# Kernel tuning notes

Hardware: AMD Instinct MI355X
Metric: run time of the kernel (lower is better)

Reference implementation:

```python
import jax, jax.numpy as jnp
import numpy as np

H = 16          # n_self_heads
CHUNK = 256     # chunk_size in chunk_gate_retention
GLN = 16.0      # gate_logit_normalizer
EPS = 1e-5      # norm_eps


def _rope_interleaved(t, cos, sin):
    # t: [B,T,H,hd]; cos,sin: [T,hd//2]; interleaved pairs (even, odd)
    x1 = t[..., 0::2]
    x2 = t[..., 1::2]
    c = cos[None, :, None, :]
    s = sin[None, :, None, :]
    r1 = x1 * c - x2 * s
    r2 = x1 * s + x2 * c
    return jnp.stack([r1, r2], axis=-1).reshape(t.shape)


def setup_inputs() -> dict:
    key = jax.random.key(0)
    ks = jax.random.split(key, 8)
    B, T, D = 2, 4096, 2048
    hd = D // H
    sc = D ** -0.5
    x = jax.random.normal(ks[0], (B, T, D), jnp.float32)
    # real rotary tables (interleaved), [T, hd//2]
    inv_freq = 1.0 / (10000.0 ** (np.arange(0, hd, 2, dtype=np.float32) / hd))
    ang = np.outer(np.arange(T, dtype=np.float32), inv_freq)
    cos = jnp.asarray(np.cos(ang))
    sin = jnp.asarray(np.sin(ang))
    Wq = jax.random.normal(ks[1], (D, D), jnp.float32) * sc
    Wk = jax.random.normal(ks[2], (D, D), jnp.float32) * sc
    Wv = jax.random.normal(ks[3], (D, D), jnp.float32) * sc
    Wg = jax.random.normal(ks[4], (D, D), jnp.float32) * sc
    Wgt = jax.random.normal(ks[5], (D, H), jnp.float32) * sc
    Wout = jax.random.normal(ks[6], (D, D), jnp.float32) * sc
    return {"x": x, "cos": cos, "sin": sin, "Wq": Wq, "Wk": Wk, "Wv": Wv,
            "Wg": Wg, "Wgt": Wgt, "Wout": Wout}


def reference(x, cos, sin, Wq, Wk, Wv, Wg, Wgt, Wout):
    B, T, D = x.shape
    hd = D // H
    N = T // CHUNK
    scale = hd ** -0.5

    q = (x @ Wq).reshape(B, T, H, hd)
    k = (x @ Wk).reshape(B, T, H, hd)
    v = (x @ Wv).reshape(B, T, H, hd)
    g = x @ Wg                                   # [B,T,D] swiglu gate
    gt = jax.nn.log_sigmoid(x @ Wgt) / GLN       # [B,T,H] log-decay per head

    q = _rope_interleaved(q, cos, sin)
    k = _rope_interleaved(k, cos, sin)

    # chunk: [B,H,N,C,hd]
    def chunked(t):
        return t.transpose(0, 2, 1, 3).reshape(B, H, N, CHUNK, hd)
    qc, kc, vc = chunked(q), chunked(k), chunked(v)

    gtc = gt.transpose(0, 2, 1).reshape(B, H, N, CHUNK).astype(jnp.float32)
    gcum = jnp.cumsum(gtc, axis=-1)              # inclusive cumsum within chunk

    # intra-chunk: A[i,j] = (q_i.k_j)*scale * exp(gcum_i - gcum_j), j <= i
    mask = jnp.tril(jnp.ones((CHUNK, CHUNK), bool))
    dec = jnp.where(mask, jnp.exp(gcum[..., :, None] - gcum[..., None, :]), 0.0).astype(x.dtype)
    scores = jnp.einsum('bhncd,bhnsd->bhncs', qc * scale, kc) * dec
    o_inner = jnp.einsum('bhncs,bhnsd->bhncd', scores, vc)

    # cross-chunk recurrent state: S <- S*exp(g_total) + (k*exp(g_total-gcum))^T V * scale
    g_tot = gcum[..., -1:]                       # [B,H,N,1]
    k_dec = jnp.exp(g_tot - gcum).astype(x.dtype)
    S_in = jnp.einsum('bhncd,bhnce->bhnde', kc * k_dec[..., None] * scale, vc)  # [B,H,N,hd,hd]
    q_dec = jnp.exp(gcum).astype(x.dtype)        # [B,H,N,C]
    chunk_dec = jnp.exp(gcum[..., -1]).astype(x.dtype)  # [B,H,N]

    def step(S, inp):
        qcn, qd, Sin, cd = inp
        o_cross = jnp.einsum('bhcd,bhde->bhce', qcn * qd[..., None], S)
        S_new = S * cd[..., None, None] + Sin
        return S_new, o_cross

    xs = (jnp.moveaxis(qc, 2, 0), jnp.moveaxis(q_dec, 2, 0),
          jnp.moveaxis(S_in, 2, 0), jnp.moveaxis(chunk_dec, 2, 0))
    S0 = jnp.zeros((B, H, hd, hd), x.dtype)
    _, o_cross = jax.lax.scan(step, S0, xs)      # [N,B,H,C,hd]

    o = o_inner + jnp.moveaxis(o_cross, 0, 2)    # [B,H,N,C,hd]
    # RMSNorm over head_dim, no affine
    o = o * jax.lax.rsqrt(jnp.mean(o * o, axis=-1, keepdims=True) + EPS)
    o = o.reshape(B, H, T, hd).transpose(0, 2, 1, 3).reshape(B, T, D)
    o = jax.nn.silu(g) * o                       # swiglu(g, o)
    return o @ Wout
```

## Files before the change

### kernel.cpp

```cpp
#include <hip/hip_runtime.h>

typedef unsigned short u16;
typedef short bf16x8 __attribute__((ext_vector_type(8)));
typedef unsigned short u16x8 __attribute__((ext_vector_type(8)));
typedef unsigned short u16x4 __attribute__((ext_vector_type(4)));
typedef float f32x4 __attribute__((ext_vector_type(4)));

typedef __attribute__((address_space(1))) void* gas_ptr;
typedef __attribute__((address_space(3))) void* las_ptr;

__device__ __forceinline__ float bf2f(u16 v) {
  unsigned u = ((unsigned)v) << 16;
  return __builtin_bit_cast(float, u);
}
__device__ __forceinline__ u16 f2bf(float f) {
  unsigned u = __builtin_bit_cast(unsigned, f);
  u += 0x7fffu + ((u >> 16) & 1u);
  return (u16)(u >> 16);
}
__device__ __forceinline__ f32x4 mfma16(bf16x8 a, bf16x8 b, f32x4 c) {
  return __builtin_amdgcn_mfma_f32_16x16x32_bf16(a, b, c, 0, 0, 0);
}
__device__ __forceinline__ void gload_lds16(const void* g, void* l) {
  __builtin_amdgcn_global_load_lds((gas_ptr)g, (las_ptr)l, 16, 0, 0);
}

#define SB __builtin_amdgcn_sched_barrier(0)
#define BAR do { SB; __builtin_amdgcn_s_barrier(); SB; } while (0)
#define LGK do { asm volatile("s_waitcnt lgkmcnt(0)" ::: "memory"); SB; } while (0)

__global__ void k_cast(const float* __restrict__ in, u16* __restrict__ out, int n8) {
  int stride = gridDim.x * blockDim.x;
  for (int i = blockIdx.x * blockDim.x + threadIdx.x; i < n8; i += stride) {
    size_t base = (size_t)i * 8;
    f32x4 a = *(const f32x4*)(in + base);
    f32x4 b = *(const f32x4*)(in + base + 4);
    u16x8 o;
    o[0] = f2bf(a[0]); o[1] = f2bf(a[1]); o[2] = f2bf(a[2]); o[3] = f2bf(a[3]);
    o[4] = f2bf(b[0]); o[5] = f2bf(b[1]); o[6] = f2bf(b[2]); o[7] = f2bf(b[3]);
    *(u16x8*)(out + base) = o;
  }
}

__global__ __launch_bounds__(256) void k_wtrans(const float* __restrict__ W, u16* __restrict__ WT,
                                                int K, int N) {
  int n0 = blockIdx.x * 64, k0 = blockIdx.y * 64;
  int tid = threadIdx.x;
  __shared__ __align__(16) float tf[64][68];
  int r = tid >> 4, c4 = (tid & 15) * 4;
#pragma unroll
  for (int i = 0; i < 4; ++i) {
    int row = r + i * 16;
    f32x4 v = *(const f32x4*)(W + (size_t)(k0 + row) * N + n0 + c4);
    *(f32x4*)&tf[row][c4] = v;
  }
  __syncthreads();
#pragma unroll
  for (int i = 0; i < 2; ++i) {
    int chunk = tid + i * 256;
    int nl = chunk >> 3, c8 = (chunk & 7) * 8;
    u16x8 o;
#pragma unroll
    for (int m = 0; m < 8; ++m) o[m] = f2bf(tf[c8 + m][nl]);
    *(u16x8*)(WT + (size_t)(n0 + nl) * K + k0 + c8) = o;
  }
}

template <int MODE>
__global__ __launch_bounds__(512, 2) void k_gemm2(const u16* __restrict__ A,
                                                  const u16* __restrict__ Bt,
                                                  void* __restrict__ Cp, int M, int N, int K) {
  __shared__ __align__(16) u16 Al[2][2][8192];
  __shared__ __align__(16) u16 Bl[2][2][8192];
  int tid = threadIdx.x, w = tid >> 6, lane = tid & 63, l15 = lane & 15, l4 = lane >> 4;
  int wm = w >> 2, wn = w & 3;
  int nwg = gridDim.x, bid = blockIdx.x;
  int q8 = nwg >> 3;
  int wg = (bid & 7) * q8 + (bid >> 3);
  int nbx = N >> 8;
  int nstx = nbx >> 2;
  int st = wg >> 4, r16 = wg & 15;
  int sm = st / nstx, sn = st - sm * nstx;
  int m0 = ((sm << 2) + (r16 >> 2)) << 8;
  int n0 = ((sn << 2) + (r16 & 3)) << 8;
  int rA0, rA1, rB0, rB1, cc0, cc1;
  {
    int rr[2], cch[2];
#pragma unroll
    for (int q = 0; q < 2; ++q) {
      int L = (q * 512 + tid) * 16;
      int sub = L >> 10, inner = L & 1023;
      inner ^= ((inner >> 9) & 1) << 5;
      rr[q] = ((sub >> 1) << 4) + (inner >> 6);
      cch[q] = ((sub & 1) << 5) + ((inner & 63) >> 1);
    }
    rA0 = ((rr[0] >> 6) << 7) + (rr[0] & 63);
    rA1 = ((rr[1] >> 6) << 7) + (rr[1] & 63);
    rB0 = ((rr[0] >> 5) << 6) + (rr[0] & 31);
    rB1 = ((rr[1] >> 5) << 6) + (rr[1] & 31);
    cc0 = cch[0]; cc1 = cch[1];
  }
  int innerA = ((l15 << 6) + (l4 << 4)) ^ ((l15 & 8) << 2);
  int ldsW = w << 9;

#define STAGE_A(t, h)                                                                   \
  do {                                                                                  \
    int b_ = (t) & 1;                                                                   \
    gload_lds16(A + (size_t)(m0 + rA0 + (h) * 64) * K + (t) * 64 + cc0, &Al[b_][h][ldsW]); \
    gload_lds16(A + (size_t)(m0 + rA1 + (h) * 64) * K + (t) * 64 + cc1, &Al[b_][h][4096 + ldsW]); \
  } while (0)
#define STAGE_B(t, h)                                                                   \
  do {                                                                                  \
    int b_ = (t) & 1;                                                                   \
    gload_lds16(Bt + (size_t)(n0 + rB0 + (h) * 32) * K + (t) * 64 + cc0, &Bl[b_][h][ldsW]); \
    gload_lds16(Bt + (size_t)(n0 + rB1 + (h) * 32) * K + (t) * 64 + cc1, &Bl[b_][h][4096 + ldsW]); \
  } while (0)

  const f32x4 z4 = {0.f, 0.f, 0.f, 0.f};
  f32x4 acc[8][4];
#pragma unroll
  for (int i = 0; i < 8; ++i)
#pragma unroll
    for (int j = 0; j < 4; ++j) acc[i][j] = z4;
  bf16x8 af[4][2], bfr[2][2];

#define LDA(cur, hm)                                                                     \
  do {                                                                                   \
    const char* Ab = (const char*)&Al[cur][hm][0];                                       \
    _Pragma("unroll") for (int fi = 0; fi < 4; ++fi) _Pragma("unroll") for (int ks = 0; ks < 2; ++ks) \
        af[fi][ks] = *(const bf16x8*)(Ab + (((wm * 4 + fi) * 2 + ks) << 10) + innerA);   \
  } while (0)
#define LDB(cur, hn)                                                                     \
  do {                                                                                   \
    const char* Bb = (const char*)&Bl[cur][hn][0];                                       \
    _Pragma("unroll") for (int fj = 0; fj < 2; ++fj) _Pragma("unroll") for (int ks = 0; ks < 2; ++ks) \
        bfr[fj][ks] = *(const bf16x8*)(Bb + (((wn * 2 + fj) * 2 + ks) << 10) + innerA);  \
  } while (0)
#define MM(hm, hn)                                                                       \
  do {                                                                                   \
    __builtin_amdgcn_s_setprio(1);                                                       \
    _Pragma("unroll") for (int fi = 0; fi < 4; ++fi) _Pragma("unroll") for (int fj = 0; fj < 2; ++fj) \
        _Pragma("unroll") for (int ks = 0; ks < 2; ++ks)                                 \
            acc[(hm) * 4 + fi][(hn) * 2 + fj] =                                          \
                mfma16(af[fi][ks], bfr[fj][ks], acc[(hm) * 4 + fi][(hn) * 2 + fj]);      \
    __builtin_amdgcn_s_setprio(0);                                                       \
  } while (0)
#define GATE8 do { asm volatile("s_waitcnt vmcnt(8)" ::: "memory"); SB; } while (0)
#define GATE0 do { asm volatile("s_waitcnt vmcnt(0)" ::: "memory"); SB; } while (0)

  int nt = K >> 6;
  STAGE_A(0, 0); STAGE_B(0, 0); STAGE_A(0, 1); STAGE_B(0, 1);
  if (nt > 1) {
    STAGE_A(1, 0); STAGE_B(1, 0);
    asm volatile("s_waitcnt vmcnt(4)" ::: "memory");
  } else {
    asm volatile("s_waitcnt vmcnt(0)" ::: "memory");
  }
  SB;
  BAR;
  for (int t = 0; t < nt; ++t) {
    int cur = t & 1;
    bool tail = (t >= nt - 2);
    LDA(cur, 0); LDB(cur, 0);
    if (t + 1 < nt) STAGE_B(t + 1, 1);
    asm volatile("s_waitcnt lgkmcnt(8)" ::: "memory");
    BAR; LGK;
    MM(0, 0);
    if (tail) GATE0; else GATE8;
    BAR;
    LDB(cur, 1);
    if (t + 1 < nt) STAGE_A(t + 1, 1);
    BAR; LGK;
    MM(0, 1);
    if (tail) GATE0; else GATE8;
    BAR;
    LDA(cur, 1); LDB(cur, 0);
    if (t + 2 < nt) STAGE_A(t + 2, 0);
    asm volatile("s_waitcnt lgkmcnt(8)" ::: "memory");
    BAR; LGK;
    MM(1, 0);
    BAR;
    LDB(cur, 1);
    if (t + 2 < nt) STAGE_B(t + 2, 0);
    BAR; LGK;
    MM(1, 1);
    if (tail) GATE0; else GATE8;
    BAR;
  }
  asm volatile("s_waitcnt vmcnt(0)" ::: "memory");
#undef STAGE_A
#undef STAGE_B
#undef LDA
#undef LDB
#undef MM
#undef GATE8
#undef GATE0
#pragma unroll
  for (int fi = 0; fi < 8; ++fi)
#pragma unroll
    for (int fj = 0; fj < 4; ++fj) {
      int row = m0 + wm * 128 + fi * 16 + l4 * 4;
      int col = n0 + wn * 64 + fj * 16 + l15;
      if (MODE == 1) {
        float* C = (float*)Cp;
#pragma unroll
        for (int reg = 0; reg < 4; ++reg) C[(size_t)(row + reg) * N + col] = acc[fi][fj][reg];
      } else {
        u16* C = (u16*)Cp + (size_t)(col >> 11) * 16777216 + (col & 2047);
#pragma unroll
        for (int reg = 0; reg < 4; ++reg) C[(size_t)(row + reg) * 2048] = f2bf(acc[fi][fj][reg]);
      }
    }
}

__global__ __launch_bounds__(256) void k_gt(const float* __restrict__ x, const float* __restrict__ Wgt,
                                            float* __restrict__ gt) {
  int t = blockIdx.x, tid = threadIdx.x;
  __shared__ __align__(16) float xs[2048];
#pragma unroll
  for (int i = 0; i < 8; ++i) xs[tid + i * 256] = x[(size_t)t * 2048 + tid + i * 256];
  __syncthreads();
  int head = tid & 15, ks = tid >> 4;
  float p = 0.f;
  for (int i = 0; i < 128; ++i) {
    int k = ks + i * 16;
    p += xs[k] * Wgt[k * 16 + head];
  }
  __shared__ float ps[16][17];
  ps[ks][head] = p;
  __syncthreads();
  if (tid < 16) {
    float z = 0.f;
#pragma unroll
    for (int j = 0; j < 16; ++j) z += ps[j][tid];
    float lsz = (z >= 0.f) ? -log1pf(__expf(-z)) : (z - log1pf(__expf(z)));
    int b = t >> 12, tl = t & 4095;
    gt[((size_t)(b * 16 + tid)) * 4096 + tl] = lsz * 0.0625f;
  }
}

__global__ void k_cumsum(const float* __restrict__ gt, float* __restrict__ gcum) {
  int n = blockIdx.x, bh = blockIdx.y, c = threadIdx.x;
  __shared__ float s[256];
  size_t base = (size_t)bh * 4096 + n * 256;
  s[c] = gt[base + c];
  __syncthreads();
  for (int off = 1; off < 256; off <<= 1) {
    float t = (c >= off) ? s[c - off] : 0.f;
    __syncthreads();
    s[c] += t;
    __syncthreads();
  }
  gcum[base + c] = s[c];
}

__global__ void k_rope(u16* __restrict__ q, u16* __restrict__ k,
                       const float* __restrict__ cosT, const float* __restrict__ sinT) {
  const size_t total = (size_t)8192 * 512;
  size_t stride = (size_t)gridDim.x * blockDim.x;
  for (size_t idx = (size_t)blockIdx.x * blockDim.x + threadIdx.x; idx < total; idx += stride) {
    size_t tok = idx >> 9;
    int g4 = (int)(idx & 511);
    int col = g4 * 4;
    int i0 = (col & 127) >> 1;
    int tl = (int)(tok & 4095);
    float c0 = cosT[tl * 64 + i0], s0 = sinT[tl * 64 + i0];
    float c1 = cosT[tl * 64 + i0 + 1], s1 = sinT[tl * 64 + i0 + 1];
    size_t base = tok * 2048 + col;
    u16x4 qv = *(u16x4*)(q + base);
    float a0 = bf2f(qv[0]), a1 = bf2f(qv[1]), a2 = bf2f(qv[2]), a3 = bf2f(qv[3]);
    u16x4 qo;
    qo[0] = f2bf(a0 * c0 - a1 * s0); qo[1] = f2bf(a0 * s0 + a1 * c0);
    qo[2] = f2bf(a2 * c1 - a3 * s1); qo[3] = f2bf(a2 * s1 + a3 * c1);
    *(u16x4*)(q + base) = qo;
    u16x4 kv = *(u16x4*)(k + base);
    float b0 = bf2f(kv[0]), b1 = bf2f(kv[1]), b2 = bf2f(kv[2]), b3 = bf2f(kv[3]);
    u16x4 ko;
    ko[0] = f2bf(b0 * c0 - b1 * s0); ko[1] = f2bf(b0 * s0 + b1 * c0);
    ko[2] = f2bf(b2 * c1 - b3 * s1); ko[3] = f2bf(b2 * s1 + b3 * c1);
    *(u16x4*)(k + base) = ko;
  }
}

__global__ __launch_bounds__(256) void k_sin(const u16* __restrict__ kb, const u16* __restrict__ vb,
                                             const float* __restrict__ gcum, float* __restrict__ SinT) {
  int n = blockIdx.x, bh = blockIdx.y;
  int b = bh >> 4, h = bh & 15;
  int tid = threadIdx.x, w = tid >> 6, lane = tid & 63, l15 = lane & 15, l4 = lane >> 4;
  size_t t0 = (size_t)b * 4096 + n * 256;
  __shared__ float gc[256];
  __shared__ __align__(16) u16 kt[128 * 72];
  __shared__ __align__(16) u16 vt[128 * 72];
  gc[tid] = gcum[(size_t)bh * 4096 + n * 256 + tid];
  __syncthreads();
  float gtot = gc[255];
  const float scale = 0.08838834764831845f;
  const f32x4 z4 = {0.f, 0.f, 0.f, 0.f};
  f32x4 acc[2][8];
#pragma unroll
  for (int i = 0; i < 2; ++i)
#pragma unroll
    for (int j = 0; j < 8; ++j) acc[i][j] = z4;
  int cl = tid >> 2, fq = (tid & 3) * 32;
  for (int c0 = 0; c0 < 256; c0 += 64) {
    __syncthreads();
    float kd = __expf(gtot - gc[c0 + cl]) * scale;
    const u16* kp = kb + (t0 + c0 + cl) * 2048 + h * 128 + fq;
    const u16* vp = vb + (t0 + c0 + cl) * 2048 + h * 128 + fq;
#pragma unroll
    for (int jj = 0; jj < 4; ++jj) {
      u16x8 kv = *(const u16x8*)(kp + jj * 8);
      u16x8 vv = *(const u16x8*)(vp + jj * 8);
#pragma unroll
      for (int m = 0; m < 8; ++m) {
        int f = fq + jj * 8 + m;
        kt[f * 72 + cl] = f2bf(bf2f(kv[m]) * kd);
        vt[f * 72 + cl] = vv[m];
      }
    }
    __syncthreads();
#pragma unroll
    for (int ks = 0; ks < 2; ++ks) {
      int coff = ks * 32 + l4 * 8;
      bf16x8 bfr[8];
#pragma unroll
      for (int bc = 0; bc < 8; ++bc) bfr[bc] = *(const bf16x8*)(vt + (bc * 16 + l15) * 72 + coff);
#pragma unroll
      for (int ar = 0; ar < 2; ++ar) {
        bf16x8 afr = *(const bf16x8*)(kt + (w * 32 + ar * 16 + l15) * 72 + coff);
#pragma unroll
        for (int bc = 0; bc < 8; ++bc) acc[ar][bc] = mfma16(afr, bfr[bc], acc[ar][bc]);
      }
    }
  }
  size_t sbo = ((size_t)bh * 16 + n) * 16384;
#pragma unroll
  for (int ar = 0; ar < 2; ++ar) {
    int d = w * 32 + ar * 16 + l4 * 4;
#pragma unroll
    for (int bc = 0; bc < 8; ++bc) {
      int e = bc * 16 + l15;
      *(f32x4*)(SinT + sbo + (size_t)e * 128 + d) = acc[ar][bc];
    }
  }
}

__global__ void k_state(const float* __restrict__ SinT, const float* __restrict__ gcum,
                        u16* __restrict__ S_T) {
  int bh = blockIdx.x >> 3, sl = blockIdx.x & 7;
  int base_l = sl * 2048 + threadIdx.x;
  float S[8];
#pragma unroll
  for (int i = 0; i < 8; ++i) S[i] = 0.f;
  for (int nn = 0; nn < 16; ++nn) {
    size_t tb = ((size_t)bh * 16 + nn) * 16384;
#pragma unroll
    for (int i = 0; i < 8; ++i) S_T[tb + base_l + i * 256] = f2bf(S[i]);
    float cd = __expf(gcum[(size_t)bh * 4096 + nn * 256 + 255]);
#pragma unroll
    for (int i = 0; i < 8; ++i) S[i] = S[i] * cd + SinT[tb + base_l + i * 256];
  }
}

__global__ __launch_bounds__(512, 4) void k_attn(
    const u16* __restrict__ qb, const u16* __restrict__ kb, const u16* __restrict__ vb,
    const u16* __restrict__ gbuf, const float* __restrict__ gcum,
    const u16* __restrict__ S_T, u16* __restrict__ ob) {
  int n = blockIdx.x, bh = blockIdx.y;
  int b = bh >> 4, h = bh & 15;
  int tid = threadIdx.x, w = tid >> 6, lane = tid & 63, l15 = lane & 15, l4 = lane >> 4;
  size_t t0 = (size_t)b * 4096 + n * 256;
  __shared__ float gc[256];
  __shared__ __align__(16) u16 vt[32768];
  __shared__ __align__(16) u16 Pb[8][512];
  if (tid < 256) gc[tid] = gcum[(size_t)bh * 4096 + n * 256 + tid];
  {
    int s = tid & 255, e0 = (tid >> 8) * 64;
    const u16* vp = vb + (t0 + s) * 2048 + h * 128 + e0;
#pragma unroll
    for (int j = 0; j < 8; ++j) {
      u16x8 vv = *(const u16x8*)(vp + j * 8);
#pragma unroll
      for (int m = 0; m < 8; ++m) {
        int e = e0 + j * 8 + m;
        vt[(e * 256 + s) ^ ((e & 7) << 3)] = vv[m];
      }
    }
  }
  __syncthreads();
  const float scale = 0.08838834764831845f;
  u16* P = Pb[w];
  const f32x4 z4 = {0.f, 0.f, 0.f, 0.f};
  f32x4 acc[2][8];
#pragma unroll
  for (int i = 0; i < 2; ++i)
#pragma unroll
    for (int j = 0; j < 8; ++j) acc[i][j] = z4;
  int r0s[2], nsbs[2];
  r0s[0] = w * 16;        nsbs[0] = (w + 2) >> 1;
  r0s[1] = (15 - w) * 16; nsbs[1] = 8 - (w >> 1);
#pragma unroll
  for (int rb = 0; rb < 2; ++rb) {
    int r0 = r0s[rb], nsb = nsbs[rb];
    bf16x8 qa[4];
    {
      const u16* qp = qb + (t0 + r0 + l15) * 2048 + h * 128 + l4 * 8;
#pragma unroll
      for (int ks = 0; ks < 4; ++ks) qa[ks] = *(const bf16x8*)(qp + ks * 32);
    }
    for (int sbk = 0; sbk < nsb; ++sbk) {
      int s0 = sbk * 32;
      f32x4 sc[2] = {z4, z4};
#pragma unroll
      for (int cf = 0; cf < 2; ++cf) {
        const u16* kp = kb + (t0 + s0 + cf * 16 + l15) * 2048 + h * 128 + l4 * 8;
#pragma unroll
        for (int ks = 0; ks < 4; ++ks)
          sc[cf] = mfma16(qa[ks], *(const bf16x8*)(kp + ks * 32), sc[cf]);
      }
#pragma unroll
      for (int cf = 0; cf < 2; ++cf) {
        int s = s0 + cf * 16 + l15;
        float gs = gc[s];
#pragma unroll
        for (int reg = 0; reg < 4; ++reg) {
          int rl = l4 * 4 + reg;
          int r = r0 + rl;
          float val = (r >= s) ? sc[cf][reg] * scale * __expf(gc[r] - gs) : 0.f;
          P[(rl * 32 + cf * 16 + l15) ^ ((rl & 3) << 3)] = f2bf(val);
        }
      }
      bf16x8 pa = *(const bf16x8*)(P + ((l15 * 32 + l4 * 8) ^ ((l15 & 3) << 3)));
#pragma unroll
      for (int bc = 0; bc < 8; ++bc) {
        int e = bc * 16 + l15;
        bf16x8 vf = *(const bf16x8*)(vt + ((e * 256 + s0 + l4 * 8) ^ ((e & 7) << 3)));
        acc[rb][bc] = mfma16(pa, vf, acc[rb][bc]);
      }
    }
  }
  size_t sbase = ((size_t)bh * 16 + n) * 16384;
#pragma unroll
  for (int rb = 0; rb < 2; ++rb) {
    int r0 = r0s[rb];
    float qd = __expf(gc[r0 + l15]);
#pragma unroll
    for (int ks = 0; ks < 4; ++ks) {
      u16x8 qu = *(const u16x8*)(qb + (t0 + r0 + l15) * 2048 + h * 128 + ks * 32 + l4 * 8);
      u16x8 ru;
#pragma unroll
      for (int m = 0; m < 8; ++m) ru[m] = f2bf(bf2f(qu[m]) * qd);
      bf16x8 pa2 = __builtin_bit_cast(bf16x8, ru);
#pragma unroll
      for (int bc = 0; bc < 8; ++bc) {
        int e = bc * 16 + l15;
        bf16x8 sf = *(const bf16x8*)(S_T + sbase + (size_t)e * 128 + ks * 32 + l4 * 8);
        acc[rb][bc] = mfma16(pa2, sf, acc[rb][bc]);
      }
    }
  }
#pragma unroll
  for (int rb = 0; rb < 2; ++rb) {
    int r0 = r0s[rb];
#pragma unroll
    for (int reg = 0; reg < 4; ++reg) {
      float ss = 0.f;
#pragma unroll
      for (int bc = 0; bc < 8; ++bc) { float v = acc[rb][bc][reg]; ss += v * v; }
      ss += __shfl_xor(ss, 1);
      ss += __shfl_xor(ss, 2);
      ss += __shfl_xor(ss, 4);
      ss += __shfl_xor(ss, 8);
      float rinv = rsqrtf(ss * 0.0078125f + 1e-5f);
      int r = r0 + l4 * 4 + reg;
      size_t rowoff = (t0 + r) * 2048 + h * 128;
#pragma unroll
      for (int bc = 0; bc < 8; ++bc) {
        int e = bc * 16 + l15;
        float gval = bf2f(gbuf[rowoff + e]);
        float sig = 1.f / (1.f + __expf(-gval));
        ob[rowoff + e] = f2bf(acc[rb][bc][reg] * rinv * gval * sig);
      }
    }
  }
}

extern "C" void kernel_launch(void* const* d_in, const int* in_sizes, int n_in,
                              void* d_out, int out_size, void* d_ws, size_t ws_size,
                              hipStream_t stream) {
  const float* x    = (const float*)d_in[0];
  const float* cosT = (const float*)d_in[1];
  const float* sinT = (const float*)d_in[2];
  const float* Wq   = (const float*)d_in[3];
  const float* Wk   = (const float*)d_in[4];
  const float* Wv   = (const float*)d_in[5];
  const float* Wg   = (const float*)d_in[6];
  const float* Wgt  = (const float*)d_in[7];
  const float* Wout = (const float*)d_in[8];
  float* out = (float*)d_out;

  const size_t MB32 = (size_t)33554432;
  const size_t W8   = (size_t)8388608;
  char* ws = (char*)d_ws;
  size_t need = MB32 + 5 * W8 + 4 * MB32 + 2 * (size_t)524288;
  if (ws_size < need) return;

  u16*   xb    = (u16*)(ws);
  float* SinT  = (float*)(ws);
  u16*   ob    = (u16*)(ws);
  u16*   WqT   = (u16*)(ws + MB32);
  u16*   S_T   = (u16*)(ws + MB32);
  u16*   WoutT = (u16*)(ws + MB32 + 4 * W8);
  u16*   qb    = (u16*)(ws + MB32 + 5 * W8);
  u16*   kb    = qb + 16777216;
  u16*   vb    = qb + 2 * 16777216;
  u16*   gb    = qb + 3 * (size_t)16777216;
  float* gt    = (float*)(ws + MB32 + 5 * W8 + 4 * MB32);
  float* gcum  = (float*)(ws + MB32 + 5 * W8 + 4 * MB32 + 524288);

  k_cast<<<2048, 256, 0, stream>>>(x, xb, 2097152);
  k_wtrans<<<dim3(32, 32), 256, 0, stream>>>(Wq, WqT, 2048, 2048);
  k_wtrans<<<dim3(32, 32), 256, 0, stream>>>(Wk, WqT + 4194304, 2048, 2048);
  k_wtrans<<<dim3(32, 32), 256, 0, stream>>>(Wv, WqT + 2 * 4194304, 2048, 2048);
  k_wtrans<<<dim3(32, 32), 256, 0, stream>>>(Wg, WqT + 3 * (size_t)4194304, 2048, 2048);
  k_wtrans<<<dim3(32, 32), 256, 0, stream>>>(Wout, WoutT, 2048, 2048);

  k_gemm2<2><<<1024, 512, 0, stream>>>(xb, WqT, qb, 8192, 8192, 2048);

  k_gt<<<8192, 256, 0, stream>>>(x, Wgt, gt);
  k_cumsum<<<dim3(16, 32), 256, 0, stream>>>(gt, gcum);
  k_rope<<<4096, 256, 0, stream>>>(qb, kb, cosT, sinT);
  k_sin<<<dim3(16, 32), 256, 0, stream>>>(kb, vb, gcum, SinT);
  k_state<<<256, 256, 0, stream>>>(SinT, gcum, S_T);
  k_attn<<<dim3(16, 32), 512, 0, stream>>>(qb, kb, vb, gb, gcum, S_T, ob);
  k_gemm2<1><<<256, 512, 0, stream>>>(ob, WoutT, out, 8192, 2048, 2048);
}
```

Before: 590.7 us.

## Keep both B halves in registers and relax GEMM pipeline waits

The GEMM main loop now holds both B-fragment halves in registers (bfr gains an hn dimension), so the B reloads from LDS before the second and fourth MFMA phases are gone. The prologue staging order and the vmcnt thresholds are reworked so global->LDS waits happen only twice per K-step, and several barriers and lgkmcnt waits are removed. This cuts LDS traffic and synchronisation per iteration at the cost of more VGPRs. It also risks a race if the new wait counts do not match the staging order.

```diff
diff --git a/kernel.cpp b/kernel.cpp
--- a/kernel.cpp
+++ b/kernel.cpp
@@ -122,7 +122,7 @@
   for (int i = 0; i < 8; ++i)
 #pragma unroll
     for (int j = 0; j < 4; ++j) acc[i][j] = z4;
-  bf16x8 af[4][2], bfr[2][2];
+  bf16x8 af[4][2], bfr[2][2][2];
 
 #define LDA(cur, hm)                                                                     \
   do {                                                                                   \
@@ -134,7 +134,7 @@
   do {                                                                                   \
     const char* Bb = (const char*)&Bl[cur][hn][0];                                       \
     _Pragma("unroll") for (int fj = 0; fj < 2; ++fj) _Pragma("unroll") for (int ks = 0; ks < 2; ++ks) \
-        bfr[fj][ks] = *(const bf16x8*)(Bb + (((wn * 2 + fj) * 2 + ks) << 10) + innerA);  \
+        bfr[hn][fj][ks] = *(const bf16x8*)(Bb + (((wn * 2 + fj) * 2 + ks) << 10) + innerA); \
   } while (0)
 #define MM(hm, hn)                                                                       \
   do {                                                                                   \
@@ -142,49 +142,43 @@
     _Pragma("unroll") for (int fi = 0; fi < 4; ++fi) _Pragma("unroll") for (int fj = 0; fj < 2; ++fj) \
         _Pragma("unroll") for (int ks = 0; ks < 2; ++ks)                                 \
             acc[(hm) * 4 + fi][(hn) * 2 + fj] =                                          \
-                mfma16(af[fi][ks], bfr[fj][ks], acc[(hm) * 4 + fi][(hn) * 2 + fj]);      \
+                mfma16(af[fi][ks], bfr[hn][fj][ks], acc[(hm) * 4 + fi][(hn) * 2 + fj]);  \
     __builtin_amdgcn_s_setprio(0);                                                       \
   } while (0)
-#define GATE8 do { asm volatile("s_waitcnt vmcnt(8)" ::: "memory"); SB; } while (0)
-#define GATE0 do { asm volatile("s_waitcnt vmcnt(0)" ::: "memory"); SB; } while (0)
 
   int nt = K >> 6;
-  STAGE_A(0, 0); STAGE_B(0, 0); STAGE_A(0, 1); STAGE_B(0, 1);
+  STAGE_A(0, 0); STAGE_B(0, 0); STAGE_B(0, 1);
   if (nt > 1) {
-    STAGE_A(1, 0); STAGE_B(1, 0);
-    asm volatile("s_waitcnt vmcnt(4)" ::: "memory");
+    STAGE_A(0, 1); STAGE_A(1, 0); STAGE_B(1, 0);
+    asm volatile("s_waitcnt vmcnt(6)" ::: "memory");
   } else {
+    STAGE_A(0, 1);
     asm volatile("s_waitcnt vmcnt(0)" ::: "memory");
   }
   SB;
   BAR;
   for (int t = 0; t < nt; ++t) {
     int cur = t & 1;
-    bool tail = (t >= nt - 2);
-    LDA(cur, 0); LDB(cur, 0);
+    LDA(cur, 0); LDB(cur, 0); LDB(cur, 1);
     if (t + 1 < nt) STAGE_B(t + 1, 1);
-    asm volatile("s_waitcnt lgkmcnt(8)" ::: "memory");
     BAR; LGK;
     MM(0, 0);
-    if (tail) GATE0; else GATE8;
     BAR;
-    LDB(cur, 1);
     if (t + 1 < nt) STAGE_A(t + 1, 1);
-    BAR; LGK;
     MM(0, 1);
-    if (tail) GATE0; else GATE8;
+    if (t < nt - 1) { asm volatile("s_waitcnt vmcnt(8)" ::: "memory"); }
+    else            { asm volatile("s_waitcnt vmcnt(0)" ::: "memory"); }
+    SB;
     BAR;
-    LDA(cur, 1); LDB(cur, 0);
+    LDA(cur, 1);
     if (t + 2 < nt) STAGE_A(t + 2, 0);
-    asm volatile("s_waitcnt lgkmcnt(8)" ::: "memory");
     BAR; LGK;
     MM(1, 0);
     BAR;
-    LDB(cur, 1);
     if (t + 2 < nt) STAGE_B(t + 2, 0);
-    BAR; LGK;
     MM(1, 1);
-    if (tail) GATE0; else GATE8;
+    if (t < nt - 2)       { asm volatile("s_waitcnt vmcnt(6)" ::: "memory"); SB; }
+    else if (t == nt - 2) { asm volatile("s_waitcnt vmcnt(2)" ::: "memory"); SB; }
     BAR;
   }
   asm volatile("s_waitcnt vmcnt(0)" ::: "memory");
@@ -193,8 +187,6 @@
 #undef LDA
 #undef LDB
 #undef MM
-#undef GATE8
-#undef GATE0
 #pragma unroll
   for (int fi = 0; fi < 8; ++fi)
 #pragma unroll
```

After: 569.4 us. -3.6%, faster.
